# Kernel tuning notes

Measured on AMD Instinct MI355X. Metric: run time of the kernel, lower is better.

Reference implementation:

```python
import jax, jax.numpy as jnp
import numpy as np

B, IMG, P, D, E, S, K, L = 2, 512, 16, 384, 768, 16, 4, 12
G = IMG // P
N = G * G  # 1024 patches

def layer_norm(x, w, b):
    m = x.mean(-1, keepdims=True)
    v = ((x - m) ** 2).mean(-1, keepdims=True)
    return (x - m) / jnp.sqrt(v + 1e-5) * w + b

def silu(x):
    return x * jax.nn.sigmoid(x)

def patch_embed(px, w, b, pos):
    Bz = px.shape[0]
    # non-overlapping patchify == stride-P conv with PxP kernel
    x = px.reshape(Bz, 3, G, P, G, P).transpose(0, 2, 4, 1, 3, 5).reshape(Bz, N, 3 * P * P)
    return x @ w.reshape(D, -1).T + b + pos

def mamba_block(x, norm_w, norm_b, in_w, in_b, conv_w, conv_b, xp_w, xp_b, dt_w, dt_b, A, Dp, out_w, out_b):
    res = x
    x = layer_norm(x, norm_w, norm_b)
    xz = x @ in_w.T + in_b                       # (B,N,2E)
    x_main, z = jnp.split(xz, 2, axis=-1)
    # depthwise causal conv (torch pads K-1 both sides then truncates to N == left pad K-1)
    xc = jax.lax.conv_general_dilated(x_main.transpose(0, 2, 1), conv_w, (1,), [(K - 1, 0)],
                                      dimension_numbers=('NCH', 'OIH', 'NCH'), feature_group_count=E)
    xc = silu((xc + conv_b[:, None]).transpose(0, 2, 1))  # (B,N,E)
    xBC = xc @ xp_w.T + xp_b
    xB, xC = jnp.split(xBC, 2, axis=-1)          # each (B,N,S)
    dt = jnp.clip(jax.nn.softplus(xB @ dt_w.T + dt_b), 1e-4, 1.0)    # (B,N,E)
    dA = jnp.exp(jnp.clip(dt[..., None] * A[None, None], -20.0, 0.0))  # (B,N,E,S)

    def step(h, inp):
        dA_i, xB_i, xC_i, xc_i = inp             # (B,E,S),(B,S),(B,S),(B,E)
        h = dA_i * h + xB_i[:, None, :] * xc_i[:, :, None]
        return h, jnp.einsum('bes,bs->be', h, xC_i)

    h0 = jnp.zeros((x.shape[0], E, S), x.dtype)
    _, ys = jax.lax.scan(step, h0, (dA.transpose(1, 0, 2, 3), xB.transpose(1, 0, 2),
                                    xC.transpose(1, 0, 2), xc.transpose(1, 0, 2)))
    y = ys.transpose(1, 0, 2)                    # (B,N,E)
    y = (y + Dp * xc) * silu(z)
    return res + y @ out_w.T + out_b

def setup_inputs() -> dict:
    key = jax.random.key(0)
    ks = jax.random.split(key, 10)
    rnd = lambda k, shape, s=0.02: jax.random.normal(k, shape, jnp.float32) * s
    return {
        'pixel_values': jax.random.normal(ks[0], (B, 3, IMG, IMG), jnp.float32),
        'patch_w': rnd(ks[1], (D, 3, P, P)),
        'patch_b': jnp.zeros((D,), jnp.float32),
        'pos_embed': rnd(ks[2], (1, N, D)),
        'norm_w': jnp.ones((L, D), jnp.float32), 'norm_b': jnp.zeros((L, D), jnp.float32),
        'in_w': rnd(ks[3], (L, 2 * E, D)), 'in_b': jnp.zeros((L, 2 * E), jnp.float32),
        'conv_w': rnd(ks[4], (L, E, 1, K), 0.3), 'conv_b': jnp.zeros((L, E), jnp.float32),
        'xp_w': rnd(ks[5], (L, 2 * S, E)), 'xp_b': jnp.zeros((L, 2 * S), jnp.float32),
        'dt_w': rnd(ks[6], (L, E, S), 0.1), 'dt_b': jnp.zeros((L, E), jnp.float32),
        'A': -jnp.tile(jnp.arange(1, S + 1, dtype=jnp.float32), (L, E, 1)),
        'Dp': jnp.ones((L, E), jnp.float32),
        'out_w': rnd(ks[7], (L, D, E)), 'out_b': jnp.zeros((L, D), jnp.float32),
        'fnorm_w': jnp.ones((D,), jnp.float32), 'fnorm_b': jnp.zeros((D,), jnp.float32),
        'scale_w': rnd(ks[8], (3, D, D)), 'scale_b': jnp.zeros((3, D), jnp.float32),
    }

def reference(pixel_values, patch_w, patch_b, pos_embed, norm_w, norm_b, in_w, in_b,
              conv_w, conv_b, xp_w, xp_b, dt_w, dt_b, A, Dp, out_w, out_b,
              fnorm_w, fnorm_b, scale_w, scale_b):
    x = patch_embed(pixel_values, patch_w, patch_b, pos_embed)
    layers_per_scale = L // 3
    scales = []
    for i in range(L):
        x = mamba_block(x, norm_w[i], norm_b[i], in_w[i], in_b[i], conv_w[i], conv_b[i],
                        xp_w[i], xp_b[i], dt_w[i], dt_b[i], A[i], Dp[i], out_w[i], out_b[i])
        if i % layers_per_scale == 0 and i // layers_per_scale < 3:
            j = i // layers_per_scale
            scales.append(x @ scale_w[j].T + scale_b[j])
    feats = layer_norm(x, fnorm_w, fnorm_b)
    # stacked: [features, scale_4, scale_8, scale_16] -> (4, B, N, D)
    return jnp.stack([feats] + scales)
```

## Files before the change

kernel.cpp:

```cpp
#include <hip/hip_runtime.h>
#include <hip/hip_bf16.h>

constexpr int Bz = 2, IMG = 512, Pp = 16, D = 384, E = 768, S = 16, L = 12;
constexpr int G = IMG / Pp;
constexpr int Np = G * G;
constexpr int M = Bz * Np;
constexpr int TWO_E = 2 * E;

typedef short bf16x8 __attribute__((ext_vector_type(8)));
typedef float fx4    __attribute__((ext_vector_type(4)));

static __device__ __forceinline__ unsigned short f2bf(float f){
  unsigned int u = __float_as_uint(f);
  u = (u + 0x7FFFu + ((u >> 16) & 1u)) >> 16;
  return (unsigned short)u;
}
static __device__ __forceinline__ float bf2f(unsigned short h){
  return __uint_as_float(((unsigned int)h) << 16);
}

static __device__ __forceinline__ float fexp2(float x){
  float r;
  asm("v_exp_f32 %0, %1" : "=v"(r) : "v"(x));
  return r;
}
static __device__ __forceinline__ float flog2(float x){
  float r;
  asm("v_log_f32 %0, %1" : "=v"(r) : "v"(x));
  return r;
}

static __device__ __forceinline__ float quad_sum(float v){
  int a = __builtin_amdgcn_update_dpp(0, __float_as_int(v), 0xB1, 0xF, 0xF, true);
  v += __int_as_float(a);
  int b = __builtin_amdgcn_update_dpp(0, __float_as_int(v), 0x4E, 0xF, 0xF, true);
  v += __int_as_float(b);
  return v;
}

constexpr size_t PW_N = (size_t)D * 768;
constexpr size_t IW_N = (size_t)L * TWO_E * D;
constexpr size_t OW_N = (size_t)L * D * E;
constexpr size_t SW_N = (size_t)3 * D * D;
__device__ short g_pw_h[PW_N], g_pw_l[PW_N];
__device__ short g_iw_h[IW_N], g_iw_l[IW_N];
__device__ short g_ow_h[OW_N], g_ow_l[OW_N];
__device__ short g_swx_h[SW_N], g_swx_l[SW_N];

__global__ void convw_kernel(const float* __restrict__ pw, const float* __restrict__ iw,
                             const float* __restrict__ ow, const float* __restrict__ sw){
  size_t i = (size_t)blockIdx.x * 256 + threadIdx.x;
  if (i >= PW_N + IW_N + OW_N + SW_N) return;
  const float* src; short *dh, *dl; size_t j = i;
  if (j < PW_N){ src = pw; dh = g_pw_h; dl = g_pw_l; }
  else if ((j -= PW_N) < IW_N){ src = iw; dh = g_iw_h; dl = g_iw_l; }
  else if ((j -= IW_N) < OW_N){ src = ow; dh = g_ow_h; dl = g_ow_l; }
  else { j -= OW_N; src = sw; dh = g_swx_h; dl = g_swx_l; }
  float f = src[j];
  unsigned short h = f2bf(f);
  dh[j] = (short)h; dl[j] = (short)f2bf(f - bf2f(h));
}

__global__ void patchify_kernel(const float* __restrict__ px,
                                short* __restrict__ oh, short* __restrict__ ol){
  int idx = blockIdx.x * 256 + threadIdx.x;
  if (idx >= M * 768) return;
  int k = idx % 768, m = idx / 768;
  int b = m / Np, n = m % Np;
  int gy = n / G, gx = n % G;
  int c = k / (Pp * Pp), r = k % (Pp * Pp);
  int py = r / Pp, pxi = r % Pp;
  size_t src = ((size_t)(b * 3 + c) * IMG + gy * Pp + py) * IMG + gx * Pp + pxi;
  float f = px[src];
  unsigned short h = f2bf(f);
  oh[idx] = (short)h; ol[idx] = (short)f2bf(f - bf2f(h));
}

__global__ __launch_bounds__(256)
void layernorm_bf(const float* __restrict__ x, const float* __restrict__ w,
                  const float* __restrict__ bb, short* __restrict__ oh,
                  short* __restrict__ ol){
  int wave = threadIdx.x >> 6, lane = threadIdx.x & 63;
  int row = blockIdx.x * 4 + wave;
  const float* xr = x + (size_t)row * D;
  float v[6], s = 0.f, sq = 0.f;
  #pragma unroll
  for (int i = 0; i < 6; i++){ v[i] = xr[lane + 64 * i]; s += v[i]; sq += v[i] * v[i]; }
  #pragma unroll
  for (int off = 32; off; off >>= 1){ s += __shfl_xor(s, off); sq += __shfl_xor(sq, off); }
  float mean = s * (1.f / D);
  float var  = sq * (1.f / D) - mean * mean;
  float inv  = 1.0f / sqrtf(var + 1e-5f);
  #pragma unroll
  for (int i = 0; i < 6; i++){
    int c = lane + 64 * i;
    float o = (v[i] - mean) * inv * w[c] + bb[c];
    unsigned short h = f2bf(o);
    oh[(size_t)row * D + c] = (short)h;
    ol[(size_t)row * D + c] = (short)f2bf(o - bf2f(h));
  }
}

__global__ __launch_bounds__(256)
void layernorm_f32(const float* __restrict__ x, const float* __restrict__ w,
                   const float* __restrict__ bb, float* __restrict__ outf){
  int wave = threadIdx.x >> 6, lane = threadIdx.x & 63;
  int row = blockIdx.x * 4 + wave;
  const float* xr = x + (size_t)row * D;
  float v[6], s = 0.f, sq = 0.f;
  #pragma unroll
  for (int i = 0; i < 6; i++){ v[i] = xr[lane + 64 * i]; s += v[i]; sq += v[i] * v[i]; }
  #pragma unroll
  for (int off = 32; off; off >>= 1){ s += __shfl_xor(s, off); sq += __shfl_xor(sq, off); }
  float mean = s * (1.f / D);
  float var  = sq * (1.f / D) - mean * mean;
  float inv  = 1.0f / sqrtf(var + 1e-5f);
  #pragma unroll
  for (int i = 0; i < 6; i++){
    int c = lane + 64 * i;
    outf[(size_t)row * D + c] = (v[i] - mean) * inv * w[c] + bb[c];
  }
}

__global__ __launch_bounds__(256)
void gemm_in(const short* __restrict__ Ah, const short* __restrict__ Al,
             size_t woff, const float* __restrict__ bias,
             float* __restrict__ C, float* __restrict__ C2){
  constexpr int BKp = 40;
  __shared__ __align__(16) short sAh[64 * BKp],  sAl[64 * BKp];
  __shared__ __align__(16) short sWh[128 * BKp], sWl[128 * BKp];
  const short* Wh = g_iw_h + woff;
  const short* Wl = g_iw_l + woff;
  const int t = threadIdx.x, wid = t >> 6, lane = t & 63;
  const int m0 = blockIdx.y * 64, n0 = blockIdx.x * 128;
  const int wn = wid * 32;

  fx4 acc[4][2];
  #pragma unroll
  for (int a = 0; a < 4; a++)
    #pragma unroll
    for (int b = 0; b < 2; b++)
      #pragma unroll
      for (int i = 0; i < 4; i++) acc[a][b][i] = 0.f;

  const int rA = t >> 2, kpA = (t & 3) << 3;
  const int rW = t >> 1, kpW = (t & 1) << 4;
  const int row = lane & 15, kq = lane >> 4;

  for (int kt = 0; kt < D; kt += 32){
    *(bf16x8*)&sAh[rA * BKp + kpA] = *(const bf16x8*)(Ah + (size_t)(m0 + rA) * D + kt + kpA);
    *(bf16x8*)&sAl[rA * BKp + kpA] = *(const bf16x8*)(Al + (size_t)(m0 + rA) * D + kt + kpA);
    *(bf16x8*)&sWh[rW * BKp + kpW]     = *(const bf16x8*)(Wh + (size_t)(n0 + rW) * D + kt + kpW);
    *(bf16x8*)&sWh[rW * BKp + kpW + 8] = *(const bf16x8*)(Wh + (size_t)(n0 + rW) * D + kt + kpW + 8);
    *(bf16x8*)&sWl[rW * BKp + kpW]     = *(const bf16x8*)(Wl + (size_t)(n0 + rW) * D + kt + kpW);
    *(bf16x8*)&sWl[rW * BKp + kpW + 8] = *(const bf16x8*)(Wl + (size_t)(n0 + rW) * D + kt + kpW + 8);
    __syncthreads();
    bf16x8 ah[4], al[4], bh[2], bl[2];
    #pragma unroll
    for (int tm = 0; tm < 4; tm++){
      ah[tm] = *(const bf16x8*)&sAh[(tm * 16 + row) * BKp + kq * 8];
      al[tm] = *(const bf16x8*)&sAl[(tm * 16 + row) * BKp + kq * 8];
    }
    #pragma unroll
    for (int tn = 0; tn < 2; tn++){
      bh[tn] = *(const bf16x8*)&sWh[(wn + tn * 16 + row) * BKp + kq * 8];
      bl[tn] = *(const bf16x8*)&sWl[(wn + tn * 16 + row) * BKp + kq * 8];
    }
    #pragma unroll
    for (int tm = 0; tm < 4; tm++)
      #pragma unroll
      for (int tn = 0; tn < 2; tn++){
        acc[tm][tn] = __builtin_amdgcn_mfma_f32_16x16x32_bf16(ah[tm], bh[tn], acc[tm][tn], 0, 0, 0);
        acc[tm][tn] = __builtin_amdgcn_mfma_f32_16x16x32_bf16(ah[tm], bl[tn], acc[tm][tn], 0, 0, 0);
        acc[tm][tn] = __builtin_amdgcn_mfma_f32_16x16x32_bf16(al[tm], bh[tn], acc[tm][tn], 0, 0, 0);
      }
    __syncthreads();
  }

  const int row4 = (lane >> 4) * 4, coln = lane & 15;
  #pragma unroll
  for (int tm = 0; tm < 4; tm++)
    #pragma unroll
    for (int tn = 0; tn < 2; tn++){
      int n = n0 + wn + tn * 16 + coln;
      int mb = m0 + tm * 16 + row4;
      float4 v4;
      float* vp = (float*)&v4;
      #pragma unroll
      for (int i = 0; i < 4; i++) vp[i] = acc[tm][tn][i] + bias[n];
      if (n < E){
        *(float4*)&C[(size_t)n * M + mb] = v4;
      } else {
        #pragma unroll
        for (int i = 0; i < 4; i++){
          float sig = 1.f / (1.f + expf(-vp[i]));
          vp[i] = vp[i] * sig;
        }
        *(float4*)&C2[(size_t)(n - E) * M + mb] = v4;
      }
    }
}

__global__ __launch_bounds__(256)
void gemm_patch(const short* __restrict__ Ah, const short* __restrict__ Al,
                const float* __restrict__ bias, float* __restrict__ C,
                const float* __restrict__ pos){
  constexpr int BKp = 40;
  __shared__ __align__(16) short sAh[64 * BKp], sAl[64 * BKp];
  __shared__ __align__(16) short sWh[64 * BKp], sWl[64 * BKp];
  const int t = threadIdx.x, wid = t >> 6, lane = t & 63;
  const int m0 = blockIdx.y * 64, n0 = blockIdx.x * 64;

  fx4 acc[4];
  #pragma unroll
  for (int a = 0; a < 4; a++)
    #pragma unroll
    for (int i = 0; i < 4; i++) acc[a][i] = 0.f;

  const int r = t >> 2, kp = (t & 3) << 3;
  const int row = lane & 15, kq = lane >> 4;

  for (int kt = 0; kt < 768; kt += 32){
    *(bf16x8*)&sAh[r * BKp + kp] = *(const bf16x8*)(Ah + (size_t)(m0 + r) * 768 + kt + kp);
    *(bf16x8*)&sAl[r * BKp + kp] = *(const bf16x8*)(Al + (size_t)(m0 + r) * 768 + kt + kp);
    *(bf16x8*)&sWh[r * BKp + kp] = *(const bf16x8*)(g_pw_h + (size_t)(n0 + r) * 768 + kt + kp);
    *(bf16x8*)&sWl[r * BKp + kp] = *(const bf16x8*)(g_pw_l + (size_t)(n0 + r) * 768 + kt + kp);
    __syncthreads();
    bf16x8 bh = *(const bf16x8*)&sWh[(wid * 16 + row) * BKp + kq * 8];
    bf16x8 bl = *(const bf16x8*)&sWl[(wid * 16 + row) * BKp + kq * 8];
    #pragma unroll
    for (int tm = 0; tm < 4; tm++){
      bf16x8 ah = *(const bf16x8*)&sAh[(tm * 16 + row) * BKp + kq * 8];
      bf16x8 al = *(const bf16x8*)&sAl[(tm * 16 + row) * BKp + kq * 8];
      acc[tm] = __builtin_amdgcn_mfma_f32_16x16x32_bf16(ah, bh, acc[tm], 0, 0, 0);
      acc[tm] = __builtin_amdgcn_mfma_f32_16x16x32_bf16(ah, bl, acc[tm], 0, 0, 0);
      acc[tm] = __builtin_amdgcn_mfma_f32_16x16x32_bf16(al, bh, acc[tm], 0, 0, 0);
    }
    __syncthreads();
  }

  const int row4 = (lane >> 4) * 4, coln = lane & 15;
  #pragma unroll
  for (int tm = 0; tm < 4; tm++){
    int n = n0 + wid * 16 + coln;
    int mb = m0 + tm * 16 + row4;
    #pragma unroll
    for (int i = 0; i < 4; i++){
      int m = mb + i;
      C[(size_t)m * D + n] = acc[tm][i] + bias[n] + pos[(size_t)(m & (Np - 1)) * D + n];
    }
  }
}

__global__ __launch_bounds__(256)
void gemm_scale(const float* __restrict__ A, size_t woff,
                const float* __restrict__ bias, float* __restrict__ C){
  constexpr int BKp = 40;
  __shared__ __align__(16) short sAh[64 * BKp], sAl[64 * BKp];
  __shared__ __align__(16) short sWh[64 * BKp], sWl[64 * BKp];
  const short* Wh = g_swx_h + woff;
  const short* Wl = g_swx_l + woff;
  const int t = threadIdx.x, wid = t >> 6, lane = t & 63;
  const int m0 = blockIdx.y * 64, n0 = blockIdx.x * 64;

  fx4 acc[4];
  #pragma unroll
  for (int a = 0; a < 4; a++)
    #pragma unroll
    for (int i = 0; i < 4; i++) acc[a][i] = 0.f;

  const int r = t >> 2, kp = (t & 3) << 3;
  const int row = lane & 15, kq = lane >> 4;

  for (int kt = 0; kt < D; kt += 32){
    {
      const float* ap = A + (size_t)(m0 + r) * D + kt + kp;
      float4 f0 = *(const float4*)ap, f1 = *(const float4*)(ap + 4);
      float f[8] = {f0.x, f0.y, f0.z, f0.w, f1.x, f1.y, f1.z, f1.w};
      short hh[8], ll[8];
      #pragma unroll
      for (int i = 0; i < 8; i++){
        unsigned short h = f2bf(f[i]);
        hh[i] = (short)h; ll[i] = (short)f2bf(f[i] - bf2f(h));
      }
      *(bf16x8*)&sAh[r * BKp + kp] = *(bf16x8*)hh;
      *(bf16x8*)&sAl[r * BKp + kp] = *(bf16x8*)ll;
    }
    *(bf16x8*)&sWh[r * BKp + kp] = *(const bf16x8*)(Wh + (size_t)(n0 + r) * D + kt + kp);
    *(bf16x8*)&sWl[r * BKp + kp] = *(const bf16x8*)(Wl + (size_t)(n0 + r) * D + kt + kp);
    __syncthreads();
    bf16x8 bh = *(const bf16x8*)&sWh[(wid * 16 + row) * BKp + kq * 8];
    bf16x8 bl = *(const bf16x8*)&sWl[(wid * 16 + row) * BKp + kq * 8];
    #pragma unroll
    for (int tm = 0; tm < 4; tm++){
      bf16x8 ah = *(const bf16x8*)&sAh[(tm * 16 + row) * BKp + kq * 8];
      bf16x8 al = *(const bf16x8*)&sAl[(tm * 16 + row) * BKp + kq * 8];
      acc[tm] = __builtin_amdgcn_mfma_f32_16x16x32_bf16(ah, bh, acc[tm], 0, 0, 0);
      acc[tm] = __builtin_amdgcn_mfma_f32_16x16x32_bf16(ah, bl, acc[tm], 0, 0, 0);
      acc[tm] = __builtin_amdgcn_mfma_f32_16x16x32_bf16(al, bh, acc[tm], 0, 0, 0);
    }
    __syncthreads();
  }

  const int row4 = (lane >> 4) * 4, coln = lane & 15;
  #pragma unroll
  for (int tm = 0; tm < 4; tm++){
    int n = n0 + wid * 16 + coln;
    int mb = m0 + tm * 16 + row4;
    #pragma unroll
    for (int i = 0; i < 4; i++){
      int m = mb + i;
      C[(size_t)m * D + n] = acc[tm][i] + bias[n];
    }
  }
}

__global__ __launch_bounds__(256)
void gemm_bf_at(const short* __restrict__ ATh, const short* __restrict__ ATl, int K,
                size_t woff, const float* __restrict__ bias,
                float* __restrict__ C, int ncols, float* __restrict__ zbuf){
  constexpr int BKp = 40;
  __shared__ __align__(16) short sAh[64 * BKp], sAl[64 * BKp];
  __shared__ __align__(16) short sWh[64 * BKp], sWl[64 * BKp];
  const short* Wh = g_ow_h + woff;
  const short* Wl = g_ow_l + woff;
  const int t = threadIdx.x, wid = t >> 6, lane = t & 63;
  const int m0 = blockIdx.y * 64, n0 = blockIdx.x * 64;

  fx4 acc[4];
  #pragma unroll
  for (int a = 0; a < 4; a++)
    #pragma unroll
    for (int i = 0; i < 4; i++) acc[a][i] = 0.f;

  const int rw = t >> 2, kpw = (t & 3) << 3;
  const int kr2 = (t & 15) * 2, mc4 = (t >> 4) * 4;
  const int row = lane & 15, kq = lane >> 4;

  for (int kt = 0; kt < K; kt += 32){
    {
      const uint2 h0 = *(const uint2*)(ATh + (size_t)(kt + kr2) * M + m0 + mc4);
      const uint2 h1 = *(const uint2*)(ATh + (size_t)(kt + kr2 + 1) * M + m0 + mc4);
      const uint2 l0 = *(const uint2*)(ATl + (size_t)(kt + kr2) * M + m0 + mc4);
      const uint2 l1 = *(const uint2*)(ATl + (size_t)(kt + kr2 + 1) * M + m0 + mc4);
      const unsigned int h0a[2] = {h0.x, h0.y}, h1a[2] = {h1.x, h1.y};
      const unsigned int l0a[2] = {l0.x, l0.y}, l1a[2] = {l1.x, l1.y};
      #pragma unroll
      for (int j = 0; j < 4; j++){
        unsigned int s0 = (h0a[j >> 1] >> ((j & 1) * 16)) & 0xFFFFu;
        unsigned int s1 = (h1a[j >> 1] >> ((j & 1) * 16)) & 0xFFFFu;
        *(unsigned int*)&sAh[(mc4 + j) * BKp + kr2] = s0 | (s1 << 16);
        unsigned int t0 = (l0a[j >> 1] >> ((j & 1) * 16)) & 0xFFFFu;
        unsigned int t1 = (l1a[j >> 1] >> ((j & 1) * 16)) & 0xFFFFu;
        *(unsigned int*)&sAl[(mc4 + j) * BKp + kr2] = t0 | (t1 << 16);
      }
    }
    *(bf16x8*)&sWh[rw * BKp + kpw] = *(const bf16x8*)(Wh + (size_t)(n0 + rw) * K + kt + kpw);
    *(bf16x8*)&sWl[rw * BKp + kpw] = *(const bf16x8*)(Wl + (size_t)(n0 + rw) * K + kt + kpw);
    __syncthreads();
    bf16x8 bh = *(const bf16x8*)&sWh[(wid * 16 + row) * BKp + kq * 8];
    bf16x8 bl = *(const bf16x8*)&sWl[(wid * 16 + row) * BKp + kq * 8];
    #pragma unroll
    for (int tm = 0; tm < 4; tm++){
      bf16x8 ah = *(const bf16x8*)&sAh[(tm * 16 + row) * BKp + kq * 8];
      bf16x8 al = *(const bf16x8*)&sAl[(tm * 16 + row) * BKp + kq * 8];
      acc[tm] = __builtin_amdgcn_mfma_f32_16x16x32_bf16(ah, bh, acc[tm], 0, 0, 0);
      acc[tm] = __builtin_amdgcn_mfma_f32_16x16x32_bf16(ah, bl, acc[tm], 0, 0, 0);
      acc[tm] = __builtin_amdgcn_mfma_f32_16x16x32_bf16(al, bh, acc[tm], 0, 0, 0);
    }
    __syncthreads();
  }

  const int row4 = (lane >> 4) * 4, coln = lane & 15;
  #pragma unroll
  for (int tm = 0; tm < 4; tm++)
    #pragma unroll
    for (int i = 0; i < 4; i++){
      int m = m0 + tm * 16 + row4 + i;
      int n = n0 + wid * 16 + coln;
      float v = acc[tm][i] + bias[n] + C[(size_t)m * ncols + n];
      C[(size_t)m * ncols + n] = v;
    }

  int gid = blockIdx.y * gridDim.x + blockIdx.x;
  int idx = gid * 256 + t;
  if (idx < M * 16)
    *(float2*)&zbuf[idx * 2] = make_float2(0.f, 0.f);
}

__global__ __launch_bounds__(256)
void gemm_xp(const float* __restrict__ xmT, const float* __restrict__ cw,
             const float* __restrict__ cb, const float* __restrict__ W,
             const float* __restrict__ bias, float* __restrict__ xcT,
             float* __restrict__ C){
  __shared__ float As[16][68];
  __shared__ float Ws[16][32 + 1];
  int tid = threadIdx.x;
  int tx = tid & 15, ty = tid >> 4;
  int m0 = blockIdx.y * 64, kb = blockIdx.x * 192;
  float acc[4][2];
  #pragma unroll
  for (int i = 0; i < 4; i++){ acc[i][0] = 0.f; acc[i][1] = 0.f; }
  for (int kt = kb; kt < kb + 192; kt += 16){
    {
      int e = kt + ty;
      int mbase = m0 + tx * 4;
      const float* src = xmT + (size_t)e * M + mbase;
      float4 cur = *(const float4*)src;
      float4 prv = make_float4(0.f, 0.f, 0.f, 0.f);
      if (mbase >= 4) prv = *(const float4*)(src - 4);
      float4 w4 = *(const float4*)(cw + e * 4);
      float cb_e = cb[e];
      float vin[8] = {prv.x, prv.y, prv.z, prv.w, cur.x, cur.y, cur.z, cur.w};
      float4 outv;
      float* op = (float*)&outv;
      #pragma unroll
      for (int j = 0; j < 4; j++){
        int m = mbase + j, n = m & (Np - 1);
        float a = cb_e + w4.w * vin[4 + j];
        if (n >= 1) a += w4.z * vin[3 + j];
        if (n >= 2) a += w4.y * vin[2 + j];
        if (n >= 3) a += w4.x * vin[1 + j];
        float sig = 1.f / (1.f + expf(-a));
        op[j] = a * sig;
      }
      *(float4*)&As[ty][tx * 4] = outv;
      *(float4*)&xcT[(size_t)e * M + mbase] = outv;
    }
    if (tid < 128){
      int c = tid >> 2, kk = (tid & 3) << 2;
      const float* wp = W + (size_t)c * E + kt + kk;
      Ws[kk + 0][c] = wp[0]; Ws[kk + 1][c] = wp[1];
      Ws[kk + 2][c] = wp[2]; Ws[kk + 3][c] = wp[3];
    }
    __syncthreads();
    #pragma unroll
    for (int k = 0; k < 16; k++){
      float a[4], w[2];
      #pragma unroll
      for (int i = 0; i < 4; i++) a[i] = As[k][ty * 4 + i];
      w[0] = Ws[k][tx * 2]; w[1] = Ws[k][tx * 2 + 1];
      #pragma unroll
      for (int i = 0; i < 4; i++){ acc[i][0] += a[i] * w[0]; acc[i][1] += a[i] * w[1]; }
    }
    __syncthreads();
  }
  #pragma unroll
  for (int i = 0; i < 4; i++){
    int m = m0 + ty * 4 + i;
    #pragma unroll
    for (int j = 0; j < 2; j++){
      int n = tx * 2 + j;
      float v = acc[i][j];
      if (blockIdx.x == 0) v += bias[n];
      atomicAdd(&C[(size_t)m * 32 + n], v);
    }
  }
}

__global__ __launch_bounds__(256)
void scan_kernel(const float* __restrict__ xcT, const float* __restrict__ zst,
                 const float* __restrict__ xBC,
                 const float* __restrict__ Aptr, const float* __restrict__ Dp,
                 const float* __restrict__ dt_w, const float* __restrict__ dt_b,
                 short* __restrict__ yh, short* __restrict__ yl){
  __shared__ float sdx[2176];
  __shared__ float sHin[64 * 16];
  __shared__ float scr[2048];
  const int t = threadIdx.x;
  const int c = t >> 2;
  const int u = t & 3;
  const int r = blockIdx.x, b = r / E, e = r % E;
  const int bNp = b * Np;
  const float dpe = Dp[e];
  constexpr float LOG2E  = 1.4426950408889634f;
  constexpr float RLOG2E = 0.6931471805599453f;
  float4 a4 = *(const float4*)(Aptr + e * S + u * 4);
  const float a20 = a4.x * LOG2E, a21 = a4.y * LOG2E, a22 = a4.z * LOG2E, a23 = a4.w * LOG2E;
  const float* xcp = xcT + (size_t)e * M + bNp;
  const float* zsp = zst + (size_t)e * M + bNp;

  {
    const float* dw = dt_w + e * 16;
    float4 w0 = *(const float4*)dw,       float4w1 = *(const float4*)(dw + 4);
    float4 w2 = *(const float4*)(dw + 8), w3 = *(const float4*)(dw + 12);
    float db = dt_b[e];
    float xcl[4];
    #pragma unroll
    for (int p = 0; p < 4; p++) xcl[p] = xcp[t + p * 256];
    float4 ra[2][4];
    {
      const float* xb0 = xBC + (size_t)(bNp + t) * 32;
      #pragma unroll
      for (int j = 0; j < 4; j++) ra[0][j] = *(const float4*)(xb0 + j * 4);
    }
    #pragma unroll
    for (int p = 0; p < 4; p++){
      int q = t + p * 256;
      float4 a0 = ra[p & 1][0], a1 = ra[p & 1][1], a2 = ra[p & 1][2], a3 = ra[p & 1][3];
      if (p < 3){
        const float* xbn = xBC + (size_t)(bNp + q + 256) * 32;
        #pragma unroll
        for (int j = 0; j < 4; j++) ra[(p + 1) & 1][j] = *(const float4*)(xbn + j * 4);
      }
      float v = db + a0.x * w0.x + a0.y * w0.y + a0.z * w0.z + a0.w * w0.w
                   + a1.x * float4w1.x + a1.y * float4w1.y + a1.z * float4w1.z + a1.w * float4w1.w
                   + a2.x * w2.x + a2.y * w2.y + a2.z * w2.z + a2.w * w2.w
                   + a3.x * w3.x + a3.y * w3.y + a3.z * w3.z + a3.w * w3.w;
      v = flog2(1.f + fexp2(v * LOG2E)) * RLOG2E;
      v = fminf(fmaxf(v, 1e-4f), 1.0f);
      int w = (q << 1) + ((q >> 4) << 1);
      *(float2*)&sdx[w] = make_float2(v, xcl[p]);
    }
  }
  __syncthreads();

  const int pos0 = c * 16;
  const int wbase = 34 * c;
  const float* xbp  = xBC + ((size_t)(bNp + pos0) * 32 + u * 4);
  const float* xcsp = xbp + 16;

  float h0 = 0.f, h1 = 0.f, h2 = 0.f, h3 = 0.f, sdt = 0.f;
  {
    float4 xbv[8];
    #pragma unroll
    for (int j = 0; j < 8; j++) xbv[j] = *(const float4*)(xbp + (size_t)j * 32);
    #pragma unroll
    for (int i = 0; i < 16; i++){
      float2 dx = *(const float2*)&sdx[wbase + 2 * i];
      float4 xb = xbv[i & 7];
      if (i < 8) xbv[i] = *(const float4*)(xbp + (size_t)(i + 8) * 32);
      float dt = dx.x, xcv = dx.y;
      sdt += dt;
      float e0 = fexp2(dt * a20), e1 = fexp2(dt * a21);
      float e2 = fexp2(dt * a22), e3 = fexp2(dt * a23);
      h0 = e0 * h0 + xb.x * xcv;
      h1 = e1 * h1 + xb.y * xcv;
      h2 = e2 * h2 + xb.z * xcv;
      h3 = e3 * h3 + xb.w * xcv;
    }
  }
  {
    float p0 = fexp2(sdt * a20), p1 = fexp2(sdt * a21);
    float p2 = fexp2(sdt * a22), p3 = fexp2(sdt * a23);
    *(float4*)&scr[c * 16 + u * 4]        = make_float4(h0, h1, h2, h3);
    *(float4*)&scr[1024 + c * 16 + u * 4] = make_float4(p0, p1, p2, p3);
  }
  __syncthreads();

  if (t < 16){
    float H = 0.f;
    #pragma unroll 8
    for (int cc = 0; cc < 64; cc++){
      sHin[cc * 16 + t] = H;
      H = scr[1024 + cc * 16 + t] * H + scr[cc * 16 + t];
    }
  }
  __syncthreads();

  float4 z4 = *(const float4*)&zsp[t * 4];

  {
    float4 hin = *(const float4*)&sHin[c * 16 + u * 4];
    h0 = hin.x; h1 = hin.y; h2 = hin.z; h3 = hin.w;
  }
  float* yloc = scr;
  const int ybase = pos0 + ((pos0 >> 4) << 2);
  {
    float4 xbv[6], xcs6[6];
    #pragma unroll
    for (int j = 0; j < 6; j++){
      xbv[j]  = *(const float4*)(xbp  + (size_t)j * 32);
      xcs6[j] = *(const float4*)(xcsp + (size_t)j * 32);
    }
    #pragma unroll
    for (int i = 0; i < 16; i++){
      float2 dx = *(const float2*)&sdx[wbase + 2 * i];
      float4 xb  = xbv[i % 6];
      float4 xcs = xcs6[i % 6];
      if (i < 10){
        xbv[i % 6]  = *(const float4*)(xbp  + (size_t)(i + 6) * 32);
        xcs6[i % 6] = *(const float4*)(xcsp + (size_t)(i + 6) * 32);
      }
      float dt = dx.x, xcv = dx.y;
      float e0 = fexp2(dt * a20), e1 = fexp2(dt * a21);
      float e2 = fexp2(dt * a22), e3 = fexp2(dt * a23);
      h0 = e0 * h0 + xb.x * xcv;
      h1 = e1 * h1 + xb.y * xcv;
      h2 = e2 * h2 + xb.z * xcv;
      h3 = e3 * h3 + xb.w * xcv;
      float yp = h0 * xcs.x + h1 * xcs.y + h2 * xcs.z + h3 * xcs.w;
      yp = quad_sum(yp);
      if (u == 0) yloc[ybase + i] = yp;
    }
  }
  __syncthreads();

  {
    int n4 = t * 4;
    const float* zp = (const float*)&z4;
    int yb = n4 + ((n4 >> 4) << 2);
    int xw = (n4 << 1) + ((n4 >> 4) << 1);
    unsigned int hpack[2], lpack[2];
    #pragma unroll
    for (int half = 0; half < 2; half++){
      unsigned int hp = 0, lp = 0;
      #pragma unroll
      for (int j = 0; j < 2; j++){
        int jj = half * 2 + j;
        float xcv = sdx[xw + 2 * jj + 1];
        float val = (yloc[yb + jj] + dpe * xcv) * zp[jj];
        unsigned short hh = f2bf(val);
        unsigned short ll = f2bf(val - bf2f(hh));
        hp |= ((unsigned int)hh) << (16 * j);
        lp |= ((unsigned int)ll) << (16 * j);
      }
      hpack[half] = hp; lpack[half] = lp;
    }
    size_t o = (size_t)e * M + bNp + n4;
    *(uint2*)&yh[o] = make_uint2(hpack[0], hpack[1]);
    *(uint2*)&yl[o] = make_uint2(lpack[0], lpack[1]);
  }
}

extern "C" void kernel_launch(void* const* d_in, const int* in_sizes, int n_in,
                              void* d_out, int out_size, void* d_ws, size_t ws_size,
                              hipStream_t stream){
  const float* px      = (const float*)d_in[0];
  const float* patch_w = (const float*)d_in[1];
  const float* patch_b = (const float*)d_in[2];
  const float* pos     = (const float*)d_in[3];
  const float* norm_w  = (const float*)d_in[4];
  const float* norm_b  = (const float*)d_in[5];
  const float* in_w    = (const float*)d_in[6];
  const float* in_b    = (const float*)d_in[7];
  const float* conv_w  = (const float*)d_in[8];
  const float* conv_b  = (const float*)d_in[9];
  const float* xp_w    = (const float*)d_in[10];
  const float* xp_b    = (const float*)d_in[11];
  const float* dt_w    = (const float*)d_in[12];
  const float* dt_b    = (const float*)d_in[13];
  const float* Aab     = (const float*)d_in[14];
  const float* Dp      = (const float*)d_in[15];
  const float* out_w   = (const float*)d_in[16];
  const float* out_b   = (const float*)d_in[17];
  const float* fnorm_w = (const float*)d_in[18];
  const float* fnorm_b = (const float*)d_in[19];
  const float* scale_w = (const float*)d_in[20];
  const float* scale_b = (const float*)d_in[21];
  float* out = (float*)d_out;

  float* x   = (float*)d_ws;
  float* xmT = x + (size_t)M * D;
  float* zst = xmT + (size_t)M * E;
  float* xcT = zst + (size_t)M * E;
  float* xBC = xcT + (size_t)M * E;
  short* xnh = (short*)(xBC + (size_t)M * 32);
  short* xnl = xnh + (size_t)M * D;
  short* yh  = (short*)xmT;
  short* yl  = yh + (size_t)M * E;
  short* pbh = yh, *pbl = yl;

  constexpr size_t TOTW = PW_N + IW_N + OW_N + SW_N;
  convw_kernel<<<(int)((TOTW + 255) / 256), 256, 0, stream>>>(patch_w, in_w, out_w, scale_w);
  hipMemsetAsync(xBC, 0, (size_t)M * 32 * sizeof(float), stream);

  patchify_kernel<<<(M * 768 + 255) / 256, 256, 0, stream>>>(px, pbh, pbl);
  gemm_patch<<<dim3(D / 64, M / 64), 256, 0, stream>>>(pbh, pbl, patch_b, x, pos);

  for (int l = 0; l < L; l++){
    layernorm_bf<<<M / 4, 256, 0, stream>>>(x, norm_w + l * D, norm_b + l * D, xnh, xnl);
    gemm_in<<<dim3(TWO_E / 128, M / 64), 256, 0, stream>>>(
        xnh, xnl, (size_t)l * TWO_E * D, in_b + l * TWO_E, xmT, zst);
    gemm_xp<<<dim3(4, M / 64), 256, 0, stream>>>(
        xmT, conv_w + (size_t)l * E * 4, conv_b + l * E,
        xp_w + (size_t)l * 32 * E, xp_b + l * 32, xcT, xBC);
    scan_kernel<<<Bz * E, 256, 0, stream>>>(
        xcT, zst, xBC, Aab + (size_t)l * E * S, Dp + l * E,
        dt_w + (size_t)l * E * S, dt_b + l * E, yh, yl);
    gemm_bf_at<<<dim3(D / 64, M / 64), 256, 0, stream>>>(
        yh, yl, E, (size_t)l * D * E, out_b + l * D, x, D, xBC);
    if (l % 4 == 0 && l / 4 < 3){
      int j = l / 4;
      gemm_scale<<<dim3(D / 64, M / 64), 256, 0, stream>>>(
          x, (size_t)j * D * D, scale_b + j * D, out + (size_t)(1 + j) * M * D);
    }
  }
  layernorm_f32<<<M / 4, 256, 0, stream>>>(x, fnorm_w, fnorm_b, out);
}
```

Measured before the change: 1.538 ms.

## Fuse layernorm into in-proj GEMM using row stats from residual epilogues

```diff
diff --git a/kernel.cpp b/kernel.cpp
--- a/kernel.cpp
+++ b/kernel.cpp
@@ -77,31 +77,6 @@
 }
 
 __global__ __launch_bounds__(256)
-void layernorm_bf(const float* __restrict__ x, const float* __restrict__ w,
-                  const float* __restrict__ bb, short* __restrict__ oh,
-                  short* __restrict__ ol){
-  int wave = threadIdx.x >> 6, lane = threadIdx.x & 63;
-  int row = blockIdx.x * 4 + wave;
-  const float* xr = x + (size_t)row * D;
-  float v[6], s = 0.f, sq = 0.f;
-  #pragma unroll
-  for (int i = 0; i < 6; i++){ v[i] = xr[lane + 64 * i]; s += v[i]; sq += v[i] * v[i]; }
-  #pragma unroll
-  for (int off = 32; off; off >>= 1){ s += __shfl_xor(s, off); sq += __shfl_xor(sq, off); }
-  float mean = s * (1.f / D);
-  float var  = sq * (1.f / D) - mean * mean;
-  float inv  = 1.0f / sqrtf(var + 1e-5f);
-  #pragma unroll
-  for (int i = 0; i < 6; i++){
-    int c = lane + 64 * i;
-    float o = (v[i] - mean) * inv * w[c] + bb[c];
-    unsigned short h = f2bf(o);
-    oh[(size_t)row * D + c] = (short)h;
-    ol[(size_t)row * D + c] = (short)f2bf(o - bf2f(h));
-  }
-}
-
-__global__ __launch_bounds__(256)
 void layernorm_f32(const float* __restrict__ x, const float* __restrict__ w,
                    const float* __restrict__ bb, float* __restrict__ outf){
   int wave = threadIdx.x >> 6, lane = threadIdx.x & 63;
@@ -123,7 +98,8 @@
 }
 
 __global__ __launch_bounds__(256)
-void gemm_in(const short* __restrict__ Ah, const short* __restrict__ Al,
+void gemm_in(const float* __restrict__ X, const float* __restrict__ rs,
+             const float* __restrict__ nw, const float* __restrict__ nb,
              size_t woff, const float* __restrict__ bias,
              float* __restrict__ C, float* __restrict__ C2){
   constexpr int BKp = 40;
@@ -147,9 +123,34 @@
   const int rW = t >> 1, kpW = (t & 1) << 4;
   const int row = lane & 15, kq = lane >> 4;
 
+  float mean, inv;
+  {
+    float s  = rs[(m0 + rA) * 2];
+    float sq = rs[(m0 + rA) * 2 + 1];
+    mean = s * (1.f / D);
+    float var = sq * (1.f / D) - mean * mean;
+    inv = 1.0f / sqrtf(var + 1e-5f);
+  }
+
   for (int kt = 0; kt < D; kt += 32){
-    *(bf16x8*)&sAh[rA * BKp + kpA] = *(const bf16x8*)(Ah + (size_t)(m0 + rA) * D + kt + kpA);
-    *(bf16x8*)&sAl[rA * BKp + kpA] = *(const bf16x8*)(Al + (size_t)(m0 + rA) * D + kt + kpA);
+    {
+      const float* xp = X + (size_t)(m0 + rA) * D + kt + kpA;
+      float4 f0 = *(const float4*)xp, f1 = *(const float4*)(xp + 4);
+      float4 wv0 = *(const float4*)(nw + kt + kpA), wv1 = *(const float4*)(nw + kt + kpA + 4);
+      float4 bv0 = *(const float4*)(nb + kt + kpA), bv1 = *(const float4*)(nb + kt + kpA + 4);
+      float f[8]  = {f0.x, f0.y, f0.z, f0.w, f1.x, f1.y, f1.z, f1.w};
+      float wv[8] = {wv0.x, wv0.y, wv0.z, wv0.w, wv1.x, wv1.y, wv1.z, wv1.w};
+      float bv[8] = {bv0.x, bv0.y, bv0.z, bv0.w, bv1.x, bv1.y, bv1.z, bv1.w};
+      short hh[8], ll[8];
+      #pragma unroll
+      for (int i2 = 0; i2 < 8; i2++){
+        float o = (f[i2] - mean) * inv * wv[i2] + bv[i2];
+        unsigned short h = f2bf(o);
+        hh[i2] = (short)h; ll[i2] = (short)f2bf(o - bf2f(h));
+      }
+      *(bf16x8*)&sAh[rA * BKp + kpA] = *(bf16x8*)hh;
+      *(bf16x8*)&sAl[rA * BKp + kpA] = *(bf16x8*)ll;
+    }
     *(bf16x8*)&sWh[rW * BKp + kpW]     = *(const bf16x8*)(Wh + (size_t)(n0 + rW) * D + kt + kpW);
     *(bf16x8*)&sWh[rW * BKp + kpW + 8] = *(const bf16x8*)(Wh + (size_t)(n0 + rW) * D + kt + kpW + 8);
     *(bf16x8*)&sWl[rW * BKp + kpW]     = *(const bf16x8*)(Wl + (size_t)(n0 + rW) * D + kt + kpW);
@@ -204,7 +205,7 @@
 __global__ __launch_bounds__(256)
 void gemm_patch(const short* __restrict__ Ah, const short* __restrict__ Al,
                 const float* __restrict__ bias, float* __restrict__ C,
-                const float* __restrict__ pos){
+                const float* __restrict__ pos, float* __restrict__ rsn){
   constexpr int BKp = 40;
   __shared__ __align__(16) short sAh[64 * BKp], sAl[64 * BKp];
   __shared__ __align__(16) short sWh[64 * BKp], sWl[64 * BKp];
@@ -247,7 +248,15 @@
     #pragma unroll
     for (int i = 0; i < 4; i++){
       int m = mb + i;
-      C[(size_t)m * D + n] = acc[tm][i] + bias[n] + pos[(size_t)(m & (Np - 1)) * D + n];
+      float v = acc[tm][i] + bias[n] + pos[(size_t)(m & (Np - 1)) * D + n];
+      C[(size_t)m * D + n] = v;
+      float s = v, sq = v * v;
+      #pragma unroll
+      for (int off = 1; off < 16; off <<= 1){ s += __shfl_xor(s, off); sq += __shfl_xor(sq, off); }
+      if ((lane & 15) == 0){
+        atomicAdd(&rsn[m * 2], s);
+        atomicAdd(&rsn[m * 2 + 1], sq);
+      }
     }
   }
 }
@@ -318,7 +327,8 @@
 __global__ __launch_bounds__(256)
 void gemm_bf_at(const short* __restrict__ ATh, const short* __restrict__ ATl, int K,
                 size_t woff, const float* __restrict__ bias,
-                float* __restrict__ C, int ncols, float* __restrict__ zbuf){
+                float* __restrict__ C, int ncols, float* __restrict__ zbuf,
+                float* __restrict__ rsn){
   constexpr int BKp = 40;
   __shared__ __align__(16) short sAh[64 * BKp], sAl[64 * BKp];
   __shared__ __align__(16) short sWh[64 * BKp], sWl[64 * BKp];
@@ -380,6 +390,13 @@
       int n = n0 + wid * 16 + coln;
       float v = acc[tm][i] + bias[n] + C[(size_t)m * ncols + n];
       C[(size_t)m * ncols + n] = v;
+      float s = v, sq = v * v;
+      #pragma unroll
+      for (int off = 1; off < 16; off <<= 1){ s += __shfl_xor(s, off); sq += __shfl_xor(sq, off); }
+      if ((lane & 15) == 0){
+        atomicAdd(&rsn[m * 2], s);
+        atomicAdd(&rsn[m * 2 + 1], sq);
+      }
     }
 
   int gid = blockIdx.y * gridDim.x + blockIdx.x;
@@ -463,7 +480,8 @@
                  const float* __restrict__ xBC,
                  const float* __restrict__ Aptr, const float* __restrict__ Dp,
                  const float* __restrict__ dt_w, const float* __restrict__ dt_b,
-                 short* __restrict__ yh, short* __restrict__ yl){
+                 short* __restrict__ yh, short* __restrict__ yl,
+                 float* __restrict__ rsz){
   __shared__ float sdx[2176];
   __shared__ float sHin[64 * 16];
   __shared__ float scr[2048];
@@ -473,6 +491,12 @@
   const int r = blockIdx.x, b = r / E, e = r % E;
   const int bNp = b * Np;
   const float dpe = Dp[e];
+
+  {
+    int gi = r * 256 + t;
+    if (gi < M * 2) rsz[gi] = 0.f;
+  }
+
   constexpr float LOG2E  = 1.4426950408889634f;
   constexpr float RLOG2E = 0.6931471805599453f;
   float4 a4 = *(const float4*)(Aptr + e * S + u * 4);
@@ -482,7 +506,7 @@
 
   {
     const float* dw = dt_w + e * 16;
-    float4 w0 = *(const float4*)dw,       float4w1 = *(const float4*)(dw + 4);
+    float4 w0 = *(const float4*)dw,       w1 = *(const float4*)(dw + 4);
     float4 w2 = *(const float4*)(dw + 8), w3 = *(const float4*)(dw + 12);
     float db = dt_b[e];
     float xcl[4];
@@ -504,7 +528,7 @@
         for (int j = 0; j < 4; j++) ra[(p + 1) & 1][j] = *(const float4*)(xbn + j * 4);
       }
       float v = db + a0.x * w0.x + a0.y * w0.y + a0.z * w0.z + a0.w * w0.w
-                   + a1.x * float4w1.x + a1.y * float4w1.y + a1.z * float4w1.z + a1.w * float4w1.w
+                   + a1.x * w1.x + a1.y * w1.y + a1.z * w1.z + a1.w * w1.w
                    + a2.x * w2.x + a2.y * w2.y + a2.z * w2.z + a2.w * w2.w
                    + a3.x * w3.x + a3.y * w3.y + a3.z * w3.z + a3.w * w3.w;
       v = flog2(1.f + fexp2(v * LOG2E)) * RLOG2E;
@@ -655,8 +679,8 @@
   float* zst = xmT + (size_t)M * E;
   float* xcT = zst + (size_t)M * E;
   float* xBC = xcT + (size_t)M * E;
-  short* xnh = (short*)(xBC + (size_t)M * 32);
-  short* xnl = xnh + (size_t)M * D;
+  float* rs0 = xBC + (size_t)M * 32;
+  float* rs1 = rs0 + (size_t)M * 2;
   short* yh  = (short*)xmT;
   short* yl  = yh + (size_t)M * E;
   short* pbh = yh, *pbl = yl;
@@ -664,22 +688,25 @@
   constexpr size_t TOTW = PW_N + IW_N + OW_N + SW_N;
   convw_kernel<<<(int)((TOTW + 255) / 256), 256, 0, stream>>>(patch_w, in_w, out_w, scale_w);
   hipMemsetAsync(xBC, 0, (size_t)M * 32 * sizeof(float), stream);
+  hipMemsetAsync(rs0, 0, (size_t)M * 2 * sizeof(float), stream);
 
   patchify_kernel<<<(M * 768 + 255) / 256, 256, 0, stream>>>(px, pbh, pbl);
-  gemm_patch<<<dim3(D / 64, M / 64), 256, 0, stream>>>(pbh, pbl, patch_b, x, pos);
+  gemm_patch<<<dim3(D / 64, M / 64), 256, 0, stream>>>(pbh, pbl, patch_b, x, pos, rs0);
 
   for (int l = 0; l < L; l++){
-    layernorm_bf<<<M / 4, 256, 0, stream>>>(x, norm_w + l * D, norm_b + l * D, xnh, xnl);
+    float* rs_in = (l & 1) ? rs1 : rs0;
+    float* rs_nx = (l & 1) ? rs0 : rs1;
     gemm_in<<<dim3(TWO_E / 128, M / 64), 256, 0, stream>>>(
-        xnh, xnl, (size_t)l * TWO_E * D, in_b + l * TWO_E, xmT, zst);
+        x, rs_in, norm_w + l * D, norm_b + l * D,
+        (size_t)l * TWO_E * D, in_b + l * TWO_E, xmT, zst);
     gemm_xp<<<dim3(4, M / 64), 256, 0, stream>>>(
         xmT, conv_w + (size_t)l * E * 4, conv_b + l * E,
         xp_w + (size_t)l * 32 * E, xp_b + l * 32, xcT, xBC);
     scan_kernel<<<Bz * E, 256, 0, stream>>>(
         xcT, zst, xBC, Aab + (size_t)l * E * S, Dp + l * E,
-        dt_w + (size_t)l * E * S, dt_b + l * E, yh, yl);
+        dt_w + (size_t)l * E * S, dt_b + l * E, yh, yl, rs_nx);
     gemm_bf_at<<<dim3(D / 64, M / 64), 256, 0, stream>>>(
-        yh, yl, E, (size_t)l * D * E, out_b + l * D, x, D, xBC);
+        yh, yl, E, (size_t)l * D * E, out_b + l * D, x, D, xBC, rs_nx);
     if (l % 4 == 0 && l / 4 < 3){
       int j = l / 4;
       gemm_scale<<<dim3(D / 64, M / 64), 256, 0, stream>>>(
```

New measurement: 1.643 ms. +6.9%, slower.
